# Performance work log

Measured on AMD Instinct MI355X. Metric: run time of the kernel, lower is better.

## Reference

```python
import jax, jax.numpy as jnp
import numpy as np

N_NODES = 50000


def _gcn_layer(x, W, b, src, dst, n_nodes):
    # x: [N, Fin] -> h: [N, Fout]
    h = x @ W
    # symmetric normalization deg^{-1/2} A_hat deg^{-1/2} (self-loops already in src/dst)
    deg = jax.ops.segment_sum(jnp.ones(src.shape[0], h.dtype), dst, num_segments=n_nodes)
    dis = jnp.where(deg > 0, jax.lax.rsqrt(deg), jnp.zeros_like(deg))
    norm = dis[src] * dis[dst]  # [E]
    msg = h[src] * norm[:, None]  # [E, Fout]
    out = jax.ops.segment_sum(msg, dst, num_segments=n_nodes)
    return out + b


def setup_inputs() -> dict:
    key = jax.random.key(0)
    k1, k2, k3, k4 = jax.random.split(key, 4)
    in_ch, hid, out_ch = 128, 128, 64
    x = jax.random.normal(k1, (N_NODES, in_ch), dtype=jnp.float32)
    edge_index = jax.random.randint(k2, (2, 800000), 0, N_NODES, dtype=jnp.int64)
    # glorot-style init for the linear weights
    W1 = jax.random.normal(k3, (in_ch, hid), dtype=jnp.float32) * (1.0 / np.sqrt(in_ch))
    b1 = jnp.zeros((hid,), dtype=jnp.float32)
    W2 = jax.random.normal(k4, (hid, out_ch), dtype=jnp.float32) * (1.0 / np.sqrt(hid))
    b2 = jnp.zeros((out_ch,), dtype=jnp.float32)
    return {"x": x, "edge_index": edge_index, "W1": W1, "b1": b1, "W2": W2, "b2": b2}


def reference(x, edge_index, W1, b1, W2, b2):
    n = x.shape[0]
    loops = jnp.arange(n, dtype=edge_index.dtype)
    src = jnp.concatenate([edge_index[0], loops])
    dst = jnp.concatenate([edge_index[1], loops])
    h = jnp.tanh(_gcn_layer(x, W1, b1, src, dst, n))
    return _gcn_layer(h, W2, b2, src, dst, n)
```

## Files before the change

kernel.cpp:

```cpp
#include <hip/hip_runtime.h>
#include <hip/hip_fp16.h>
#include <math.h>


__global__ __launch_bounds__(256) void normalize_kernel(const int* __restrict__ ei32,
                                                        int* __restrict__ out, int n2,
                                                        int* __restrict__ hist, int nh) {
    __shared__ int s_is64;
    if (threadIdx.x == 0) {
        int is64 = 1;
        for (int k = 1; k < 64; k += 2)
            if (ei32[k] != 0) { is64 = 0; break; }
        s_is64 = is64;
    }
    __syncthreads();
    const int is64 = s_is64;
    for (int i = blockIdx.x * blockDim.x + threadIdx.x; i < n2;
         i += gridDim.x * blockDim.x) {
        out[i] = is64 ? ei32[2 * i] : ei32[i];
        if (i < nh) hist[i] = 0;
    }
}

__global__ __launch_bounds__(256) void hist_kernel(const int* __restrict__ dst, int E,
                                                   int* __restrict__ hist) {
    for (int i = blockIdx.x * blockDim.x + threadIdx.x; i < E;
         i += gridDim.x * blockDim.x) {
        atomicAdd(&hist[dst[i]], 1);
    }
}

__global__ __launch_bounds__(256) void scan1_kernel(const int* __restrict__ hist,
                                                    int* __restrict__ row_start,
                                                    int* __restrict__ partial, int n) {
    __shared__ int tmp[256];
    int t = threadIdx.x;
    int i = blockIdx.x * 256 + t;
    int v = (i < n) ? hist[i] : 0;
    tmp[t] = v;
    __syncthreads();
    for (int off = 1; off < 256; off <<= 1) {
        int add = (t >= off) ? tmp[t - off] : 0;
        __syncthreads();
        tmp[t] += add;
        __syncthreads();
    }
    if (i < n) row_start[i] = tmp[t] - v;
    if (t == 255) partial[blockIdx.x] = tmp[255];
}

__global__ __launch_bounds__(256) void scan2_kernel(const int* __restrict__ partial,
                                                    int* __restrict__ offsets, int nb) {
    __shared__ int tmp[256];
    int t = threadIdx.x;
    int v = (t < nb) ? partial[t] : 0;
    tmp[t] = v;
    __syncthreads();
    for (int off = 1; off < 256; off <<= 1) {
        int add = (t >= off) ? tmp[t - off] : 0;
        __syncthreads();
        tmp[t] += add;
        __syncthreads();
    }
    if (t < nb) offsets[t] = tmp[t] - v;
}

__global__ __launch_bounds__(256) void scan3_kernel(int* __restrict__ row_start,
                                                    const int* __restrict__ offsets,
                                                    const int* __restrict__ hist,
                                                    float* __restrict__ dis,
                                                    int* __restrict__ cursor,
                                                    int n, int E) {
    int i = blockIdx.x * 256 + threadIdx.x;
    if (i < n) {
        row_start[i] += offsets[i >> 8];
        dis[i] = rsqrtf((float)(hist[i] + 1));
        cursor[i] = 0;
    }
    if (i == 0) row_start[n] = E;
}

__global__ __launch_bounds__(256) void scatter_kernel(const int* __restrict__ src,
                                                      const int* __restrict__ dst, int E,
                                                      const int* __restrict__ row_start,
                                                      int* __restrict__ cursor,
                                                      int* __restrict__ csr_src) {
    for (int i = blockIdx.x * blockDim.x + threadIdx.x; i < E;
         i += gridDim.x * blockDim.x) {
        int d = dst[i];
        int pos = atomicAdd(&cursor[d], 1);
        csr_src[row_start[d] + pos] = src[i];
    }
}

template <int BM, int BN, int TM, int TN, bool HALF_OUT>
__global__ __launch_bounds__(256) void gemm_tile(const float* __restrict__ A,
                                                 const float* __restrict__ B,
                                                 const float* __restrict__ scale,
                                                 void* __restrict__ Cv,
                                                 int M, int K, int N) {
    constexpr int BK = 32;
    constexpr int TX = BN / TN;
    constexpr int TY = BM / TM;
    static_assert(TX * TY == 256, "256 threads");
    const int t = threadIdx.x;
    const int tx = t % TX;
    const int ty = t / TX;
    const int row0 = blockIdx.x * BM;

    __shared__ float As[BK][BM + 4];
    __shared__ float Bs[BK][BN + 4];

    float acc[TM][TN];
#pragma unroll
    for (int i = 0; i < TM; i++)
#pragma unroll
        for (int j = 0; j < TN; j++) acc[i][j] = 0.f;

    for (int k0 = 0; k0 < K; k0 += BK) {
        constexpr int A4 = BM * BK / 4;
#pragma unroll
        for (int idx4 = t; idx4 < A4; idx4 += 256) {
            int r = idx4 / (BK / 4);
            int c4 = idx4 % (BK / 4);
            float4 v = make_float4(0.f, 0.f, 0.f, 0.f);
            int gr = row0 + r;
            if (gr < M) v = *(const float4*)&A[(size_t)gr * K + k0 + c4 * 4];
            As[c4 * 4 + 0][r] = v.x;
            As[c4 * 4 + 1][r] = v.y;
            As[c4 * 4 + 2][r] = v.z;
            As[c4 * 4 + 3][r] = v.w;
        }
        constexpr int B4 = BK * BN / 4;
#pragma unroll
        for (int idx4 = t; idx4 < B4; idx4 += 256) {
            int r = idx4 / (BN / 4);
            int c4 = idx4 % (BN / 4);
            float4 v = *(const float4*)&B[(size_t)(k0 + r) * N + c4 * 4];
            *(float4*)&Bs[r][c4 * 4] = v;
        }
        __syncthreads();

#pragma unroll 4
        for (int kk = 0; kk < BK; kk++) {
            float a[TM], b[TN];
#pragma unroll
            for (int i = 0; i < TM; i += 4)
                *(float4*)&a[i] = *(const float4*)&As[kk][ty * TM + i];
#pragma unroll
            for (int j = 0; j < TN; j += 4)
                *(float4*)&b[j] = *(const float4*)&Bs[kk][tx * TN + j];
#pragma unroll
            for (int i = 0; i < TM; i++)
#pragma unroll
                for (int j = 0; j < TN; j++) acc[i][j] += a[i] * b[j];
        }
        __syncthreads();
    }

#pragma unroll
    for (int i = 0; i < TM; i++) {
        int gr = row0 + ty * TM + i;
        if (gr < M) {
            float sc = scale[gr];
            if constexpr (HALF_OUT) {
                __half* C = (__half*)Cv;
                __half2 tmp[TN / 2];
#pragma unroll
                for (int j = 0; j < TN; j += 2)
                    tmp[j / 2] = __floats2half2_rn(acc[i][j] * sc, acc[i][j + 1] * sc);
                if constexpr (TN == 8) {
                    *(float4*)&C[(size_t)gr * N + tx * TN] = *(float4*)tmp;
                } else {
                    *(float2*)&C[(size_t)gr * N + tx * TN] = *(float2*)tmp;
                }
            } else {
                float* C = (float*)Cv;
#pragma unroll
                for (int j = 0; j < TN; j += 4) {
                    float4 v = make_float4(acc[i][j] * sc, acc[i][j + 1] * sc,
                                           acc[i][j + 2] * sc, acc[i][j + 3] * sc);
                    *(float4*)&C[(size_t)gr * N + tx * TN + j] = v;
                }
            }
        }
    }
}

__global__ __launch_bounds__(256) void agg1_kernel(const __half* __restrict__ hs,
                                                   const float* __restrict__ dis,
                                                   const int* __restrict__ row_start,
                                                   const int* __restrict__ csr_src,
                                                   const float* __restrict__ b1,
                                                   float* __restrict__ hout, int n) {
    const int wid = threadIdx.x >> 6;
    const int lane = threadIdx.x & 63;
    const __half2* hv = (const __half2*)hs;

    for (int node = blockIdx.x * 4 + wid; node < n; node += gridDim.x * 4) {
        float2 acc = __half22float2(hv[(size_t)node * 64 + lane]);

        int e0 = row_start[node], e1 = row_start[node + 1];
        int e = e0;
        for (; e + 4 <= e1; e += 4) {
            int s0 = csr_src[e + 0];
            int s1 = csr_src[e + 1];
            int s2 = csr_src[e + 2];
            int s3 = csr_src[e + 3];
            float2 v0 = __half22float2(hv[(size_t)s0 * 64 + lane]);
            float2 v1 = __half22float2(hv[(size_t)s1 * 64 + lane]);
            float2 v2 = __half22float2(hv[(size_t)s2 * 64 + lane]);
            float2 v3 = __half22float2(hv[(size_t)s3 * 64 + lane]);
            acc.x += (v0.x + v1.x) + (v2.x + v3.x);
            acc.y += (v0.y + v1.y) + (v2.y + v3.y);
        }
        for (; e < e1; ++e) {
            float2 v = __half22float2(hv[(size_t)csr_src[e] * 64 + lane]);
            acc.x += v.x;
            acc.y += v.y;
        }
        float dd = dis[node];
        float2 bb = ((const float2*)b1)[lane];
        float2 o;
        o.x = tanhf(acc.x * dd + bb.x);
        o.y = tanhf(acc.y * dd + bb.y);
        ((float2*)hout)[(size_t)node * 64 + lane] = o;
    }
}

__global__ __launch_bounds__(256) void agg2_kernel(const __half* __restrict__ hs,
                                                   const float* __restrict__ dis,
                                                   const int* __restrict__ row_start,
                                                   const int* __restrict__ csr_src,
                                                   const float* __restrict__ b2,
                                                   float* __restrict__ out, int n) {
    const int wid = threadIdx.x >> 6;
    const int lane = threadIdx.x & 63;

    for (int node = blockIdx.x * 4 + wid; node < n; node += gridDim.x * 4) {
        float acc = __half2float(hs[(size_t)node * 64 + lane]);

        int e0 = row_start[node], e1 = row_start[node + 1];
        int e = e0;
        for (; e + 4 <= e1; e += 4) {
            int s0 = csr_src[e + 0];
            int s1 = csr_src[e + 1];
            int s2 = csr_src[e + 2];
            int s3 = csr_src[e + 3];
            float v0 = __half2float(hs[(size_t)s0 * 64 + lane]);
            float v1 = __half2float(hs[(size_t)s1 * 64 + lane]);
            float v2 = __half2float(hs[(size_t)s2 * 64 + lane]);
            float v3 = __half2float(hs[(size_t)s3 * 64 + lane]);
            acc += (v0 + v1) + (v2 + v3);
        }
        for (; e < e1; ++e) {
            acc += __half2float(hs[(size_t)csr_src[e] * 64 + lane]);
        }
        out[(size_t)node * 64 + lane] = acc * dis[node] + b2[lane];
    }
}

extern "C" void kernel_launch(void* const* d_in, const int* in_sizes, int n_in,
                              void* d_out, int out_size, void* d_ws, size_t ws_size,
                              hipStream_t stream) {
    const float* x  = (const float*)d_in[0];
    const int*   ei = (const int*)d_in[1];
    const float* W1 = (const float*)d_in[2];
    const float* b1 = (const float*)d_in[3];
    const float* W2 = (const float*)d_in[4];
    const float* b2 = (const float*)d_in[5];

    const int hid    = in_sizes[3];
    const int in_ch  = in_sizes[2] / hid;
    const int out_ch = in_sizes[5];
    const int N      = in_sizes[0] / in_ch;
    const int E      = in_sizes[1] / 2;

    char* wsp = (char*)d_ws;
    auto alloc = [&](size_t bytes) -> char* {
        char* p = wsp;
        wsp += (bytes + 255) & ~(size_t)255;
        return p;
    };
    __half* h1       = (__half*)alloc((size_t)N * hid * 2);
    float*  hmid     = (float*)alloc((size_t)N * hid * 4);
    __half* h2       = (__half*)alloc((size_t)N * out_ch * 2);
    int*   hist      = (int*)alloc((size_t)N * 4);
    int*   cursor    = (int*)alloc((size_t)N * 4);
    int*   row_start = (int*)alloc((size_t)(N + 1) * 4);
    float* dis       = (float*)alloc((size_t)N * 4);
    int*   partial   = (int*)alloc(1024);
    int*   offsets   = (int*)alloc(1024);
    int*   enorm     = (int*)alloc((size_t)2 * E * 4);
    int*   csr_src   = (int*)alloc((size_t)E * 4);

    const int NB = (N + 255) / 256;

    normalize_kernel<<<2048, 256, 0, stream>>>(ei, enorm, 2 * E, hist, N);
    const int* esrc = enorm;
    const int* edst = enorm + E;

    hist_kernel<<<1024, 256, 0, stream>>>(edst, E, hist);
    scan1_kernel<<<NB, 256, 0, stream>>>(hist, row_start, partial, N);
    scan2_kernel<<<1, 256, 0, stream>>>(partial, offsets, NB);
    scan3_kernel<<<NB, 256, 0, stream>>>(row_start, offsets, hist, dis, cursor, N, E);
    scatter_kernel<<<1024, 256, 0, stream>>>(esrc, edst, E, row_start, cursor, csr_src);

    gemm_tile<128, 128, 8, 8, true><<<(N + 127) / 128, 256, 0, stream>>>(
        x, W1, dis, h1, N, in_ch, hid);
    agg1_kernel<<<1280, 256, 0, stream>>>(h1, dis, row_start, csr_src, b1, hmid, N);

    gemm_tile<128, 64, 8, 4, true><<<(N + 127) / 128, 256, 0, stream>>>(
        hmid, W2, dis, h2, N, hid, out_ch);
    agg2_kernel<<<1280, 256, 0, stream>>>(h2, dis, row_start, csr_src, b2,
                                          (float*)d_out, N);
}
```

Baseline: 314.9 us.

## Load neighbor indices cooperatively with wave shuffles and merge scan kernels

The aggregation kernels now have each lane load one CSR neighbor index per 64-edge chunk and broadcast it with __shfl, with the gather unrolled by 8. This replaces the old scheme where every lane redundantly loaded the same index, and it allows more gathers in flight. The second and third scan kernels are merged into one: every block redundantly rescans the block partials, which saves a launch. Aggregation grid sizes also go from 1280 to 2048 blocks. Average degree is about 17, so most nodes need only one chunk, and the shuffles add some instruction overhead.

```diff
diff --git a/kernel.cpp b/kernel.cpp
--- a/kernel.cpp
+++ b/kernel.cpp
@@ -49,31 +49,31 @@
     if (t == 255) partial[blockIdx.x] = tmp[255];
 }
 
-__global__ __launch_bounds__(256) void scan2_kernel(const int* __restrict__ partial,
-                                                    int* __restrict__ offsets, int nb) {
-    __shared__ int tmp[256];
+__global__ __launch_bounds__(256) void scan23_kernel(int* __restrict__ row_start,
+                                                     const int* __restrict__ partial,
+                                                     const int* __restrict__ hist,
+                                                     float* __restrict__ dis,
+                                                     int* __restrict__ cursor,
+                                                     int n, int E, int nb) {
+    __shared__ int offs[256];
     int t = threadIdx.x;
     int v = (t < nb) ? partial[t] : 0;
-    tmp[t] = v;
+    offs[t] = v;
     __syncthreads();
     for (int off = 1; off < 256; off <<= 1) {
-        int add = (t >= off) ? tmp[t - off] : 0;
-        __syncthreads();
-        tmp[t] += add;
-        __syncthreads();
-    }
-    if (t < nb) offsets[t] = tmp[t] - v;
-}
-
-__global__ __launch_bounds__(256) void scan3_kernel(int* __restrict__ row_start,
-                                                    const int* __restrict__ offsets,
-                                                    const int* __restrict__ hist,
-                                                    float* __restrict__ dis,
-                                                    int* __restrict__ cursor,
-                                                    int n, int E) {
-    int i = blockIdx.x * 256 + threadIdx.x;
+        int add = (t >= off) ? offs[t - off] : 0;
+        __syncthreads();
+        offs[t] += add;
+        __syncthreads();
+    }
+    int incl = offs[t];
+    __syncthreads();
+    offs[t] = incl - v;
+    __syncthreads();
+
+    int i = blockIdx.x * 256 + t;
     if (i < n) {
-        row_start[i] += offsets[i >> 8];
+        row_start[i] += offs[i >> 8];
         dis[i] = rsqrtf((float)(hist[i] + 1));
         cursor[i] = 0;
     }
@@ -200,24 +200,41 @@
     for (int node = blockIdx.x * 4 + wid; node < n; node += gridDim.x * 4) {
         float2 acc = __half22float2(hv[(size_t)node * 64 + lane]);
 
-        int e0 = row_start[node], e1 = row_start[node + 1];
-        int e = e0;
-        for (; e + 4 <= e1; e += 4) {
-            int s0 = csr_src[e + 0];
-            int s1 = csr_src[e + 1];
-            int s2 = csr_src[e + 2];
-            int s3 = csr_src[e + 3];
-            float2 v0 = __half22float2(hv[(size_t)s0 * 64 + lane]);
-            float2 v1 = __half22float2(hv[(size_t)s1 * 64 + lane]);
-            float2 v2 = __half22float2(hv[(size_t)s2 * 64 + lane]);
-            float2 v3 = __half22float2(hv[(size_t)s3 * 64 + lane]);
-            acc.x += (v0.x + v1.x) + (v2.x + v3.x);
-            acc.y += (v0.y + v1.y) + (v2.y + v3.y);
-        }
-        for (; e < e1; ++e) {
-            float2 v = __half22float2(hv[(size_t)csr_src[e] * 64 + lane]);
-            acc.x += v.x;
-            acc.y += v.y;
+        const int e0 = row_start[node];
+        const int deg = row_start[node + 1] - e0;
+
+        for (int base = 0; base < deg; base += 64) {
+            const int cnt = min(64, deg - base);
+            int myidx = 0;
+            if (lane < cnt) myidx = csr_src[e0 + base + lane];
+
+            int k = 0;
+            for (; k + 8 <= cnt; k += 8) {
+                int s0 = __shfl(myidx, k + 0);
+                int s1 = __shfl(myidx, k + 1);
+                int s2 = __shfl(myidx, k + 2);
+                int s3 = __shfl(myidx, k + 3);
+                int s4 = __shfl(myidx, k + 4);
+                int s5 = __shfl(myidx, k + 5);
+                int s6 = __shfl(myidx, k + 6);
+                int s7 = __shfl(myidx, k + 7);
+                float2 v0 = __half22float2(hv[(size_t)s0 * 64 + lane]);
+                float2 v1 = __half22float2(hv[(size_t)s1 * 64 + lane]);
+                float2 v2 = __half22float2(hv[(size_t)s2 * 64 + lane]);
+                float2 v3 = __half22float2(hv[(size_t)s3 * 64 + lane]);
+                float2 v4 = __half22float2(hv[(size_t)s4 * 64 + lane]);
+                float2 v5 = __half22float2(hv[(size_t)s5 * 64 + lane]);
+                float2 v6 = __half22float2(hv[(size_t)s6 * 64 + lane]);
+                float2 v7 = __half22float2(hv[(size_t)s7 * 64 + lane]);
+                acc.x += ((v0.x + v1.x) + (v2.x + v3.x)) + ((v4.x + v5.x) + (v6.x + v7.x));
+                acc.y += ((v0.y + v1.y) + (v2.y + v3.y)) + ((v4.y + v5.y) + (v6.y + v7.y));
+            }
+            for (; k < cnt; ++k) {
+                int s = __shfl(myidx, k);
+                float2 v = __half22float2(hv[(size_t)s * 64 + lane]);
+                acc.x += v.x;
+                acc.y += v.y;
+            }
         }
         float dd = dis[node];
         float2 bb = ((const float2*)b1)[lane];
@@ -240,21 +257,38 @@
     for (int node = blockIdx.x * 4 + wid; node < n; node += gridDim.x * 4) {
         float acc = __half2float(hs[(size_t)node * 64 + lane]);
 
-        int e0 = row_start[node], e1 = row_start[node + 1];
-        int e = e0;
-        for (; e + 4 <= e1; e += 4) {
-            int s0 = csr_src[e + 0];
-            int s1 = csr_src[e + 1];
-            int s2 = csr_src[e + 2];
-            int s3 = csr_src[e + 3];
-            float v0 = __half2float(hs[(size_t)s0 * 64 + lane]);
-            float v1 = __half2float(hs[(size_t)s1 * 64 + lane]);
-            float v2 = __half2float(hs[(size_t)s2 * 64 + lane]);
-            float v3 = __half2float(hs[(size_t)s3 * 64 + lane]);
-            acc += (v0 + v1) + (v2 + v3);
-        }
-        for (; e < e1; ++e) {
-            acc += __half2float(hs[(size_t)csr_src[e] * 64 + lane]);
+        const int e0 = row_start[node];
+        const int deg = row_start[node + 1] - e0;
+
+        for (int base = 0; base < deg; base += 64) {
+            const int cnt = min(64, deg - base);
+            int myidx = 0;
+            if (lane < cnt) myidx = csr_src[e0 + base + lane];
+
+            int k = 0;
+            for (; k + 8 <= cnt; k += 8) {
+                int s0 = __shfl(myidx, k + 0);
+                int s1 = __shfl(myidx, k + 1);
+                int s2 = __shfl(myidx, k + 2);
+                int s3 = __shfl(myidx, k + 3);
+                int s4 = __shfl(myidx, k + 4);
+                int s5 = __shfl(myidx, k + 5);
+                int s6 = __shfl(myidx, k + 6);
+                int s7 = __shfl(myidx, k + 7);
+                float v0 = __half2float(hs[(size_t)s0 * 64 + lane]);
+                float v1 = __half2float(hs[(size_t)s1 * 64 + lane]);
+                float v2 = __half2float(hs[(size_t)s2 * 64 + lane]);
+                float v3 = __half2float(hs[(size_t)s3 * 64 + lane]);
+                float v4 = __half2float(hs[(size_t)s4 * 64 + lane]);
+                float v5 = __half2float(hs[(size_t)s5 * 64 + lane]);
+                float v6 = __half2float(hs[(size_t)s6 * 64 + lane]);
+                float v7 = __half2float(hs[(size_t)s7 * 64 + lane]);
+                acc += ((v0 + v1) + (v2 + v3)) + ((v4 + v5) + (v6 + v7));
+            }
+            for (; k < cnt; ++k) {
+                int s = __shfl(myidx, k);
+                acc += __half2float(hs[(size_t)s * 64 + lane]);
+            }
         }
         out[(size_t)node * 64 + lane] = acc * dis[node] + b2[lane];
     }
@@ -290,7 +324,6 @@
     int*   row_start = (int*)alloc((size_t)(N + 1) * 4);
     float* dis       = (float*)alloc((size_t)N * 4);
     int*   partial   = (int*)alloc(1024);
-    int*   offsets   = (int*)alloc(1024);
     int*   enorm     = (int*)alloc((size_t)2 * E * 4);
     int*   csr_src   = (int*)alloc((size_t)E * 4);
 
@@ -302,16 +335,15 @@
 
     hist_kernel<<<1024, 256, 0, stream>>>(edst, E, hist);
     scan1_kernel<<<NB, 256, 0, stream>>>(hist, row_start, partial, N);
-    scan2_kernel<<<1, 256, 0, stream>>>(partial, offsets, NB);
-    scan3_kernel<<<NB, 256, 0, stream>>>(row_start, offsets, hist, dis, cursor, N, E);
+    scan23_kernel<<<NB, 256, 0, stream>>>(row_start, partial, hist, dis, cursor, N, E, NB);
     scatter_kernel<<<1024, 256, 0, stream>>>(esrc, edst, E, row_start, cursor, csr_src);
 
     gemm_tile<128, 128, 8, 8, true><<<(N + 127) / 128, 256, 0, stream>>>(
         x, W1, dis, h1, N, in_ch, hid);
-    agg1_kernel<<<1280, 256, 0, stream>>>(h1, dis, row_start, csr_src, b1, hmid, N);
+    agg1_kernel<<<2048, 256, 0, stream>>>(h1, dis, row_start, csr_src, b1, hmid, N);
 
     gemm_tile<128, 64, 8, 4, true><<<(N + 127) / 128, 256, 0, stream>>>(
         hmid, W2, dis, h2, N, hid, out_ch);
-    agg2_kernel<<<1280, 256, 0, stream>>>(h2, dis, row_start, csr_src, b2,
+    agg2_kernel<<<2048, 256, 0, stream>>>(h2, dis, row_start, csr_src, b2,
                                           (float*)d_out, N);
 }
```

Result: faster. 275.7 us (-12.5%).
